# Performance work log

Hardware: AMD Instinct MI355X
Metric: run time of the kernel (lower is better)

## Reference

```python
import jax, jax.numpy as jnp
import numpy as np

N, DEG = 50000, 16
E = N * DEG
F_IN, HID, F_OUT, IJ = 128, 128, 128, 16


def _mlp2(x, W1, b1, W2, b2, tanh_out):
    y = jnp.tanh(x @ W1 + b1) @ W2 + b2
    return jnp.tanh(y) if tanh_out else y


def setup_inputs() -> dict:
    key = jax.random.key(0)
    ks = jax.random.split(key, 16)
    p = lambda k, sh: jax.random.normal(k, sh, dtype=jnp.float32) * 0.05
    inp = {
        "h": jax.random.normal(ks[0], (N, F_IN), dtype=jnp.float32),
        "x": jax.random.normal(ks[1], (N, 3), dtype=jnp.float32),
        "velocidade": jax.random.normal(ks[2], (N, 3), dtype=jnp.float32),
        "atributos_arestas": jax.random.normal(ks[3], (E, IJ), dtype=jnp.float32),
        "rows": jnp.repeat(jnp.arange(N, dtype=jnp.int32), DEG),
        "cols": jax.random.randint(ks[4], (E,), 0, N, dtype=jnp.int32),
        # phi_e: Linear(2F+1+IJ, HID), Tanh, Linear(HID, HID), Tanh
        "We1": p(ks[5], (2 * F_IN + 1 + IJ, HID)), "be1": jnp.zeros(HID, jnp.float32),
        "We2": p(ks[6], (HID, HID)), "be2": jnp.zeros(HID, jnp.float32),
        # phi_x: Linear(HID, HID), Tanh, Linear(HID, 1), Tanh
        "Wx1": p(ks[7], (HID, HID)), "bx1": jnp.zeros(HID, jnp.float32),
        "Wx2": p(ks[8], (HID, 1)), "bx2": jnp.zeros(1, jnp.float32),
        # phi_h: Linear(HID+1, HID), Tanh, Linear(HID, F_OUT)
        "Wh1": p(ks[9], (HID + 1, HID)), "bh1": jnp.zeros(HID, jnp.float32),
        "Wh2": p(ks[10], (HID, F_OUT)), "bh2": jnp.zeros(F_OUT, jnp.float32),
        # phi_v: Linear(F_IN, HID), Tanh, Linear(HID, 1)
        "Wv1": p(ks[11], (F_IN, HID)), "bv1": jnp.zeros(HID, jnp.float32),
        "Wv2": p(ks[12], (HID, 1)), "bv2": jnp.zeros(1, jnp.float32),
    }
    return inp


def reference(h, x, velocidade, atributos_arestas, rows, cols,
              We1, be1, We2, be2, Wx1, bx1, Wx2, bx2,
              Wh1, bh1, Wh2, bh2, Wv1, bv1, Wv2, bv2):
    n = h.shape[0]
    diff = x[rows] - x[cols]                              # [E, 3]
    dif_radial = jnp.sum(diff * diff, axis=1, keepdims=True)  # [E, 1]
    attrs = jnp.concatenate([h[rows], h[cols], dif_radial, atributos_arestas], axis=1)
    m_ij = _mlp2(attrs, We1, be1, We2, be2, tanh_out=True)    # [E, HID]
    phi_x = _mlp2(m_ij, Wx1, bx1, Wx2, bx2, tanh_out=True)    # [E, 1]
    phi_v = _mlp2(h, Wv1, bv1, Wv2, bv2, tanh_out=False)      # [N, 1]

    counts = jax.ops.segment_sum(jnp.ones_like(rows, dtype=diff.dtype), rows, num_segments=n)

    # media_segmentada: for edge (i=rows, j=cols): acc[i] += sum_over_features(edge_tensor[j])
    # (NOTE: indexes the EDGE tensor by the column NODE id j, faithful to source)
    ex = diff * phi_x                                     # [E, 3]
    vals = jnp.sum(ex[cols], axis=1)                      # [E]
    media = jax.ops.segment_sum(vals, rows, num_segments=n)
    media = jnp.where(counts > 0, media / counts, 0.0)[:, None]  # [N, 1]

    velocidade_new = velocidade * phi_v + media           # [N, 3]
    x_new = x + velocidade_new

    # soma_segmentada on m_ij with same quirky indexing
    m_vals = jnp.sum(m_ij[cols], axis=1)                  # [E]
    m_i = jax.ops.segment_sum(m_vals, rows, num_segments=n)[:, None]  # [N, 1]

    h_new = _mlp2(jnp.concatenate([h, m_i], axis=1), Wh1, bh1, Wh2, bh2, tanh_out=False)
    return h_new, x_new, velocidade_new
```

## Files before the change

kernel.cpp:

```cpp
#include <hip/hip_runtime.h>
#include <hip/hip_bf16.h>

#define NN      50000
#define DEG     16
#define FDIM    128
#define ASTR    296
#define OSTR    136
#define OFF_WE1 0
#define OFF_WE2 36864
#define OFF_WX1 53248
#define OFF_WV1 69632
#define OFF_WH1 86016
#define OFF_WH2 102400
#define WS_SHORTS 118784

typedef short v8s  __attribute__((ext_vector_type(8)));
typedef short v4sh __attribute__((ext_vector_type(4)));
typedef short v2sh __attribute__((ext_vector_type(2)));
typedef float v4f  __attribute__((ext_vector_type(4)));

__device__ __forceinline__ float fast_tanh(float xv) {
    float ax = fabsf(xv);
    float e2 = __expf(2.0f * ax);
    float r  = 1.0f - 2.0f / (e2 + 1.0f);
    return copysignf(r, xv);
}

__device__ __forceinline__ short f2bf(float f) {
    union { float f; unsigned u; } a; a.f = f;
    unsigned r = a.u + 0x7fffu + ((a.u >> 16) & 1u);
    return (short)(unsigned short)(r >> 16);
}
__device__ __forceinline__ float bf2f(short s) {
    union { unsigned u; float f; } a; a.u = ((unsigned)(unsigned short)s) << 16;
    return a.f;
}

__device__ __forceinline__ float wave_reduce_add(float v) {
#pragma unroll
    for (int m = 32; m >= 1; m >>= 1) v += __shfl_xor(v, m, 64);
    return v;
}

template<int KSTEPS, int ASTRIDE, int KPAD>
__device__ __forceinline__ void mfma_acc(
    const short* A, const short* __restrict__ Wt, int l, int w, v4f acc[2][2])
{
    const int lm = l & 15, lk = l >> 4;
    const short* a0p = A + lm * ASTRIDE + lk * 8;
    const short* a1p = a0p + 16 * ASTRIDE;
    const short* b0p = Wt + (w * 32 + lm) * KPAD + lk * 8;
    const short* b1p = b0p + 16 * KPAD;
#pragma unroll
    for (int ks = 0; ks < KSTEPS; ++ks) {
        v8s a0 = *(const v8s*)(a0p + ks * 32);
        v8s a1 = *(const v8s*)(a1p + ks * 32);
        v8s b0 = *(const v8s*)(b0p + ks * 32);
        v8s b1 = *(const v8s*)(b1p + ks * 32);
        acc[0][0] = __builtin_amdgcn_mfma_f32_16x16x32_bf16(a0, b0, acc[0][0], 0, 0, 0);
        acc[1][0] = __builtin_amdgcn_mfma_f32_16x16x32_bf16(a1, b0, acc[1][0], 0, 0, 0);
        acc[0][1] = __builtin_amdgcn_mfma_f32_16x16x32_bf16(a0, b1, acc[0][1], 0, 0, 0);
        acc[1][1] = __builtin_amdgcn_mfma_f32_16x16x32_bf16(a1, b1, acc[1][1], 0, 0, 0);
    }
}

__device__ __forceinline__ void acc_zero(v4f acc[2][2]) {
    v4f z = {0.f, 0.f, 0.f, 0.f};
    acc[0][0] = z; acc[0][1] = z; acc[1][0] = z; acc[1][1] = z;
}

__device__ __forceinline__ void epi_to_lds(
    v4f acc[2][2], short* O, const float* __restrict__ b, int l, int w)
{
    const int rl = (l >> 4) * 4, cl = l & 15;
#pragma unroll
    for (int nt = 0; nt < 2; ++nt) {
        const int col = w * 32 + nt * 16 + cl;
        const float bias = b[col];
#pragma unroll
        for (int mt = 0; mt < 2; ++mt) {
#pragma unroll
            for (int r = 0; r < 4; ++r) {
                float v = fast_tanh(acc[mt][nt][r] + bias);
                O[(mt * 16 + rl + r) * OSTR + col] = f2bf(v);
            }
        }
    }
}

__global__ __launch_bounds__(256) void prep_weights(
    const float* __restrict__ We1, const float* __restrict__ We2,
    const float* __restrict__ Wx1, const float* __restrict__ Wv1,
    const float* __restrict__ Wh1, const float* __restrict__ Wh2,
    short* __restrict__ wbuf)
{
    int idx = blockIdx.x * 256 + threadIdx.x;
    if (idx < 128 * 288) {
        int c = idx / 288, k = idx % 288;
        wbuf[OFF_WE1 + idx] = (k < 273) ? f2bf(We1[k * FDIM + c]) : (short)0;
        return;
    }
    idx -= 128 * 288;
    if (idx < 5 * 16384) {
        int layer = idx / 16384, r = idx % 16384;
        int c = r / 128, k = r % 128;
        const float* W = (layer == 0) ? We2 : (layer == 1) ? Wx1 :
                         (layer == 2) ? Wv1 : (layer == 3) ? Wh1 : Wh2;
        wbuf[OFF_WE2 + layer * 16384 + c * 128 + k] = f2bf(W[k * FDIM + c]);
    }
}

__global__ __launch_bounds__(256) void edge_kernel(
    const float* __restrict__ h, const float* __restrict__ x,
    const float* __restrict__ ea, const int* __restrict__ cols,
    const short* __restrict__ wbuf,
    const float* __restrict__ be1, const float* __restrict__ be2,
    const float* __restrict__ bx1,
    const float* __restrict__ Wx2, const float* __restrict__ bx2,
    float* __restrict__ msum, float* __restrict__ exsum)
{
    __shared__ __align__(16) short attrs[32 * ASTR];
    __shared__ __align__(16) short buf1[32 * OSTR];
    __shared__ __align__(16) short buf2[32 * OSTR];
    __shared__ float sdiff[32];

    const int tid = threadIdx.x;
    const int e0  = blockIdx.x * 32;
    const int l   = tid & 63, w = tid >> 6, eb = w * 8;

    {
        const int el = tid >> 3, q = tid & 7;
        int ec = e0 + el; if (ec >= NN) ec = NN - 1;
        const int i = ec >> 4;
        const int j = cols[ec];
        const float4* hi4 = (const float4*)(h + (size_t)i * FDIM);
        const float4* hj4 = (const float4*)(h + (size_t)j * FDIM);
        short* arow = attrs + el * ASTR;
#pragma unroll
        for (int t = 0; t < 4; ++t) {
            float4 v = hi4[q * 4 + t];
            v4sh s = { f2bf(v.x), f2bf(v.y), f2bf(v.z), f2bf(v.w) };
            *(v4sh*)(arow + q * 16 + t * 4) = s;
            float4 u = hj4[q * 4 + t];
            v4sh s2 = { f2bf(u.x), f2bf(u.y), f2bf(u.z), f2bf(u.w) };
            *(v4sh*)(arow + 128 + q * 16 + t * 4) = s2;
        }
        if (q < 2) {
#pragma unroll
            for (int t = 0; t < 8; ++t)
                arow[257 + q * 8 + t] = f2bf(ea[(size_t)ec * 16 + q * 8 + t]);
        }
        if (q == 2) {
            float dx = x[i * 3 + 0] - x[j * 3 + 0];
            float dy = x[i * 3 + 1] - x[j * 3 + 1];
            float dz = x[i * 3 + 2] - x[j * 3 + 2];
            arow[256] = f2bf(dx * dx + dy * dy + dz * dz);
            sdiff[el] = dx + dy + dz;
        }
        if (q == 3) {
#pragma unroll
            for (int t = 0; t < 15; ++t) arow[273 + t] = 0;
        }
    }
    __syncthreads();

    v4f acc[2][2];
    acc_zero(acc);
    mfma_acc<9, ASTR, 288>(attrs, wbuf + OFF_WE1, l, w, acc);
    epi_to_lds(acc, buf1, be1, l, w);
    __syncthreads();

    acc_zero(acc);
    mfma_acc<4, OSTR, 128>(buf1, wbuf + OFF_WE2, l, w, acc);
    epi_to_lds(acc, buf2, be2, l, w);
    __syncthreads();

#pragma unroll
    for (int e = 0; e < 8; ++e) {
        int row = eb + e;
        v2sh p = *(const v2sh*)(buf2 + row * OSTR + 2 * l);
        float s = bf2f(p.x) + bf2f(p.y);
        s = wave_reduce_add(s);
        if (l == 0) {
            int eg = e0 + row;
            if (eg < NN) msum[eg] = s;
        }
    }

    acc_zero(acc);
    mfma_acc<4, OSTR, 128>(buf2, wbuf + OFF_WX1, l, w, acc);
    epi_to_lds(acc, buf1, bx1, l, w);
    __syncthreads();

    {
        const float wx0 = Wx2[2 * l], wx1 = Wx2[2 * l + 1];
        const float bxx = bx2[0];
#pragma unroll
        for (int e = 0; e < 8; ++e) {
            int row = eb + e;
            v2sh p = *(const v2sh*)(buf1 + row * OSTR + 2 * l);
            float s = bf2f(p.x) * wx0 + bf2f(p.y) * wx1;
            s = wave_reduce_add(s);
            if (l == 0) {
                int eg = e0 + row;
                if (eg < NN) exsum[eg] = fast_tanh(s + bxx) * sdiff[row];
            }
        }
    }
}

__global__ __launch_bounds__(256) void node_kernel(
    const float* __restrict__ h, const float* __restrict__ x,
    const float* __restrict__ vel, const int* __restrict__ cols,
    const short* __restrict__ wbuf,
    const float* __restrict__ bv1, const float* __restrict__ Wv2,
    const float* __restrict__ bv2,
    const float* __restrict__ bh1, const float* __restrict__ Wh1f,
    const float* __restrict__ bh2,
    const float* __restrict__ msum, const float* __restrict__ exsum,
    float* __restrict__ out_h, float* __restrict__ out_x, float* __restrict__ out_v)
{
    __shared__ __align__(16) short hn[32 * OSTR];
    __shared__ __align__(16) short buf1[32 * OSTR];
    __shared__ float mi[32], media[32], phiv[32];

    const int tid = threadIdx.x;
    const int n0  = blockIdx.x * 32;
    const int l   = tid & 63, w = tid >> 6, eb = w * 8;

    {
        const int el = tid >> 3, q = tid & 7;
        int nc = n0 + el; if (nc >= NN) nc = NN - 1;
        const float4* hr = (const float4*)(h + (size_t)nc * FDIM);
        short* arow = hn + el * OSTR;
#pragma unroll
        for (int t = 0; t < 4; ++t) {
            float4 v = hr[q * 4 + t];
            v4sh s = { f2bf(v.x), f2bf(v.y), f2bf(v.z), f2bf(v.w) };
            *(v4sh*)(arow + q * 16 + t * 4) = s;
        }
    }
    {
#pragma unroll
        for (int r = 0; r < 2; ++r) {
            int idx = tid + r * 256;
            int nl = idx >> 4, kk = idx & 15;
            int nc = n0 + nl; if (nc >= NN) nc = NN - 1;
            int c = cols[(size_t)nc * DEG + kk];
            float ms = msum[c];
            float ex = exsum[c];
#pragma unroll
            for (int m = 8; m >= 1; m >>= 1) {
                ms += __shfl_xor(ms, m, 64);
                ex += __shfl_xor(ex, m, 64);
            }
            if (kk == 0) { mi[nl] = ms; media[nl] = ex * (1.0f / 16.0f); }
        }
    }
    __syncthreads();

    v4f acc[2][2];
    acc_zero(acc);
    mfma_acc<4, OSTR, 128>(hn, wbuf + OFF_WV1, l, w, acc);
    epi_to_lds(acc, buf1, bv1, l, w);
    __syncthreads();

    {
        const float wv0 = Wv2[2 * l], wv1 = Wv2[2 * l + 1];
        const float bvv = bv2[0];
#pragma unroll
        for (int e = 0; e < 8; ++e) {
            int row = eb + e;
            v2sh p = *(const v2sh*)(buf1 + row * OSTR + 2 * l);
            float s = bf2f(p.x) * wv0 + bf2f(p.y) * wv1;
            s = wave_reduce_add(s);
            if (l == 0) phiv[row] = s + bvv;
        }
    }
    __syncthreads();

    acc_zero(acc);
    mfma_acc<4, OSTR, 128>(hn, wbuf + OFF_WH1, l, w, acc);
    {
        const int rl = (l >> 4) * 4, cl = l & 15;
        const float* w128 = Wh1f + (size_t)FDIM * FDIM;
#pragma unroll
        for (int nt = 0; nt < 2; ++nt) {
            const int col = w * 32 + nt * 16 + cl;
            const float bias = bh1[col], wr = w128[col];
#pragma unroll
            for (int mt = 0; mt < 2; ++mt) {
#pragma unroll
                for (int r = 0; r < 4; ++r) {
                    int row = mt * 16 + rl + r;
                    float v = fast_tanh(acc[mt][nt][r] + bias + mi[row] * wr);
                    buf1[row * OSTR + col] = f2bf(v);
                }
            }
        }
    }
    __syncthreads();

    acc_zero(acc);
    mfma_acc<4, OSTR, 128>(buf1, wbuf + OFF_WH2, l, w, acc);
    {
        const int rl = (l >> 4) * 4, cl = l & 15;
#pragma unroll
        for (int nt = 0; nt < 2; ++nt) {
            const int col = w * 32 + nt * 16 + cl;
            const float bias = bh2[col];
#pragma unroll
            for (int mt = 0; mt < 2; ++mt) {
#pragma unroll
                for (int r = 0; r < 4; ++r) {
                    int rg = n0 + mt * 16 + rl + r;
                    if (rg < NN) out_h[(size_t)rg * FDIM + col] = acc[mt][nt][r] + bias;
                }
            }
        }
    }

    if (tid < 96) {
        int nl = tid / 3, d = tid % 3;
        int n = n0 + nl;
        if (n < NN) {
            float vv = vel[(size_t)n * 3 + d] * phiv[nl] + media[nl];
            out_v[(size_t)n * 3 + d] = vv;
            out_x[(size_t)n * 3 + d] = x[(size_t)n * 3 + d] + vv;
        }
    }
}

extern "C" void kernel_launch(void* const* d_in, const int* in_sizes, int n_in,
                              void* d_out, int out_size, void* d_ws, size_t ws_size,
                              hipStream_t stream)
{
    (void)in_sizes; (void)n_in; (void)out_size; (void)ws_size;
    const float* h    = (const float*)d_in[0];
    const float* x    = (const float*)d_in[1];
    const float* vel  = (const float*)d_in[2];
    const float* ea   = (const float*)d_in[3];
    const int*   cols = (const int*)d_in[5];
    const float* We1 = (const float*)d_in[6];  const float* be1 = (const float*)d_in[7];
    const float* We2 = (const float*)d_in[8];  const float* be2 = (const float*)d_in[9];
    const float* Wx1 = (const float*)d_in[10]; const float* bx1 = (const float*)d_in[11];
    const float* Wx2 = (const float*)d_in[12]; const float* bx2 = (const float*)d_in[13];
    const float* Wh1 = (const float*)d_in[14]; const float* bh1 = (const float*)d_in[15];
    const float* Wh2 = (const float*)d_in[16]; const float* bh2 = (const float*)d_in[17];
    const float* Wv1 = (const float*)d_in[18]; const float* bv1 = (const float*)d_in[19];
    const float* Wv2 = (const float*)d_in[20]; const float* bv2 = (const float*)d_in[21];

    short* wbuf  = (short*)d_ws;
    float* msum  = (float*)((char*)d_ws + WS_SHORTS * sizeof(short));
    float* exsum = msum + NN;
    float* out_h = (float*)d_out;
    float* out_x = out_h + (size_t)NN * FDIM;
    float* out_v = out_x + (size_t)NN * 3;

    dim3 block(256);
    prep_weights<<<dim3((WS_SHORTS + 255) / 256), block, 0, stream>>>(
        We1, We2, Wx1, Wv1, Wh1, Wh2, wbuf);
    dim3 grid((NN + 31) / 32);
    edge_kernel<<<grid, block, 0, stream>>>(h, x, ea, cols, wbuf,
                                            be1, be2, bx1, Wx2, bx2, msum, exsum);
    node_kernel<<<grid, block, 0, stream>>>(h, x, vel, cols, wbuf,
                                            bv1, Wv2, bv2, bh1, Wh1, bh2,
                                            msum, exsum, out_h, out_x, out_v);
}
```

Measured before the change: 212.8 us.

## Double row tile to 64 and hold weight fragments in registers

Each block now processes 64 rows instead of 32, and each wave preloads its B (weight) fragments into registers once per layer. The next layer's weights are fetched while the current layer's epilogue runs. This amortizes weight loads over more rows and cuts redundant global/LDS traffic. The attrs and second hidden buffer share LDS to limit shared memory growth. In exchange register pressure rises sharply (36 B fragments for the first layer) and the grid halves, which may reduce occupancy or parallelism.

```diff
diff --git a/kernel.cpp b/kernel.cpp
--- a/kernel.cpp
+++ b/kernel.cpp
@@ -4,6 +4,7 @@
 #define NN      50000
 #define DEG     16
 #define FDIM    128
+#define BM      64
 #define ASTR    296
 #define OSTR    136
 #define OFF_WE1 0
@@ -36,41 +37,47 @@
     return a.f;
 }
 
-__device__ __forceinline__ float wave_reduce_add(float v) {
-#pragma unroll
-    for (int m = 32; m >= 1; m >>= 1) v += __shfl_xor(v, m, 64);
-    return v;
-}
-
-template<int KSTEPS, int ASTRIDE, int KPAD>
-__device__ __forceinline__ void mfma_acc(
-    const short* A, const short* __restrict__ Wt, int l, int w, v4f acc[2][2])
+template<int KSTEPS, int KPAD>
+__device__ __forceinline__ void load_B(const short* __restrict__ Wt, int l, int w,
+                                       v8s B[KSTEPS][2])
 {
     const int lm = l & 15, lk = l >> 4;
-    const short* a0p = A + lm * ASTRIDE + lk * 8;
-    const short* a1p = a0p + 16 * ASTRIDE;
-    const short* b0p = Wt + (w * 32 + lm) * KPAD + lk * 8;
-    const short* b1p = b0p + 16 * KPAD;
+    const short* b0 = Wt + (size_t)(w * 32 + lm) * KPAD + lk * 8;
 #pragma unroll
     for (int ks = 0; ks < KSTEPS; ++ks) {
-        v8s a0 = *(const v8s*)(a0p + ks * 32);
-        v8s a1 = *(const v8s*)(a1p + ks * 32);
-        v8s b0 = *(const v8s*)(b0p + ks * 32);
-        v8s b1 = *(const v8s*)(b1p + ks * 32);
-        acc[0][0] = __builtin_amdgcn_mfma_f32_16x16x32_bf16(a0, b0, acc[0][0], 0, 0, 0);
-        acc[1][0] = __builtin_amdgcn_mfma_f32_16x16x32_bf16(a1, b0, acc[1][0], 0, 0, 0);
-        acc[0][1] = __builtin_amdgcn_mfma_f32_16x16x32_bf16(a0, b1, acc[0][1], 0, 0, 0);
-        acc[1][1] = __builtin_amdgcn_mfma_f32_16x16x32_bf16(a1, b1, acc[1][1], 0, 0, 0);
-    }
-}
-
-__device__ __forceinline__ void acc_zero(v4f acc[2][2]) {
+        B[ks][0] = *(const v8s*)(b0 + ks * 32);
+        B[ks][1] = *(const v8s*)(b0 + 16 * KPAD + ks * 32);
+    }
+}
+
+__device__ __forceinline__ void acc_zero(v4f acc[4][2]) {
     v4f z = {0.f, 0.f, 0.f, 0.f};
-    acc[0][0] = z; acc[0][1] = z; acc[1][0] = z; acc[1][1] = z;
-}
-
-__device__ __forceinline__ void epi_to_lds(
-    v4f acc[2][2], short* O, const float* __restrict__ b, int l, int w)
+#pragma unroll
+    for (int mt = 0; mt < 4; ++mt) { acc[mt][0] = z; acc[mt][1] = z; }
+}
+
+template<int KSTEPS, int ASTRIDE>
+__device__ __forceinline__ void mfma_acc(const short* A, const v8s B[KSTEPS][2],
+                                         int l, v4f acc[4][2])
+{
+    const int lm = l & 15, lk = l >> 4;
+    const short* ap = A + lm * ASTRIDE + lk * 8;
+#pragma unroll
+    for (int ks = 0; ks < KSTEPS; ++ks) {
+        v8s a[4];
+#pragma unroll
+        for (int mt = 0; mt < 4; ++mt)
+            a[mt] = *(const v8s*)(ap + mt * 16 * ASTRIDE + ks * 32);
+#pragma unroll
+        for (int mt = 0; mt < 4; ++mt) {
+            acc[mt][0] = __builtin_amdgcn_mfma_f32_16x16x32_bf16(a[mt], B[ks][0], acc[mt][0], 0, 0, 0);
+            acc[mt][1] = __builtin_amdgcn_mfma_f32_16x16x32_bf16(a[mt], B[ks][1], acc[mt][1], 0, 0, 0);
+        }
+    }
+}
+
+__device__ __forceinline__ void epi_to_lds(v4f acc[4][2], short* O,
+                                           const float* __restrict__ b, int l, int w)
 {
     const int rl = (l >> 4) * 4, cl = l & 15;
 #pragma unroll
@@ -78,13 +85,10 @@
         const int col = w * 32 + nt * 16 + cl;
         const float bias = b[col];
 #pragma unroll
-        for (int mt = 0; mt < 2; ++mt) {
-#pragma unroll
-            for (int r = 0; r < 4; ++r) {
-                float v = fast_tanh(acc[mt][nt][r] + bias);
-                O[(mt * 16 + rl + r) * OSTR + col] = f2bf(v);
-            }
-        }
+        for (int mt = 0; mt < 4; ++mt)
+#pragma unroll
+            for (int r = 0; r < 4; ++r)
+                O[(mt * 16 + rl + r) * OSTR + col] = f2bf(fast_tanh(acc[mt][nt][r] + bias));
     }
 }
 
@@ -110,7 +114,7 @@
     }
 }
 
-__global__ __launch_bounds__(256) void edge_kernel(
+__global__ __launch_bounds__(256, 2) void edge_kernel(
     const float* __restrict__ h, const float* __restrict__ x,
     const float* __restrict__ ea, const int* __restrict__ cols,
     const short* __restrict__ wbuf,
@@ -119,68 +123,78 @@
     const float* __restrict__ Wx2, const float* __restrict__ bx2,
     float* __restrict__ msum, float* __restrict__ exsum)
 {
-    __shared__ __align__(16) short attrs[32 * ASTR];
-    __shared__ __align__(16) short buf1[32 * OSTR];
-    __shared__ __align__(16) short buf2[32 * OSTR];
-    __shared__ float sdiff[32];
+    __shared__ __align__(16) short bigbuf[BM * ASTR];
+    __shared__ __align__(16) short buf1[BM * OSTR];
+    __shared__ float sdiff[BM];
+
+    short* attrs = bigbuf;
+    short* buf2  = bigbuf;
 
     const int tid = threadIdx.x;
-    const int e0  = blockIdx.x * 32;
-    const int l   = tid & 63, w = tid >> 6, eb = w * 8;
-
-    {
-        const int el = tid >> 3, q = tid & 7;
+    const int e0  = blockIdx.x * BM;
+    const int l   = tid & 63, w = tid >> 6;
+
+    v8s B1[9][2];
+    load_B<9, 288>(wbuf + OFF_WE1, l, w, B1);
+
+    {
+        const int el = tid >> 2, q = tid & 3;
         int ec = e0 + el; if (ec >= NN) ec = NN - 1;
         const int i = ec >> 4;
         const int j = cols[ec];
-        const float4* hi4 = (const float4*)(h + (size_t)i * FDIM);
-        const float4* hj4 = (const float4*)(h + (size_t)j * FDIM);
+        const float4* hi4 = (const float4*)(h + (size_t)i * FDIM) + q * 8;
+        const float4* hj4 = (const float4*)(h + (size_t)j * FDIM) + q * 8;
         short* arow = attrs + el * ASTR;
 #pragma unroll
-        for (int t = 0; t < 4; ++t) {
-            float4 v = hi4[q * 4 + t];
+        for (int t = 0; t < 8; ++t) {
+            float4 v = hi4[t];
             v4sh s = { f2bf(v.x), f2bf(v.y), f2bf(v.z), f2bf(v.w) };
-            *(v4sh*)(arow + q * 16 + t * 4) = s;
-            float4 u = hj4[q * 4 + t];
+            *(v4sh*)(arow + q * 32 + t * 4) = s;
+            float4 u = hj4[t];
             v4sh s2 = { f2bf(u.x), f2bf(u.y), f2bf(u.z), f2bf(u.w) };
-            *(v4sh*)(arow + 128 + q * 16 + t * 4) = s2;
-        }
-        if (q < 2) {
-#pragma unroll
-            for (int t = 0; t < 8; ++t)
-                arow[257 + q * 8 + t] = f2bf(ea[(size_t)ec * 16 + q * 8 + t]);
-        }
-        if (q == 2) {
+            *(v4sh*)(arow + 128 + q * 32 + t * 4) = s2;
+        }
+        if (q == 0) {
+#pragma unroll
+            for (int t = 0; t < 16; ++t)
+                arow[257 + t] = f2bf(ea[(size_t)ec * 16 + t]);
+        }
+        if (q == 1) {
             float dx = x[i * 3 + 0] - x[j * 3 + 0];
             float dy = x[i * 3 + 1] - x[j * 3 + 1];
             float dz = x[i * 3 + 2] - x[j * 3 + 2];
             arow[256] = f2bf(dx * dx + dy * dy + dz * dz);
             sdiff[el] = dx + dy + dz;
         }
-        if (q == 3) {
+        if (q == 2) {
 #pragma unroll
             for (int t = 0; t < 15; ++t) arow[273 + t] = 0;
         }
     }
     __syncthreads();
 
-    v4f acc[2][2];
-    acc_zero(acc);
-    mfma_acc<9, ASTR, 288>(attrs, wbuf + OFF_WE1, l, w, acc);
+    v4f acc[4][2];
+    acc_zero(acc);
+    mfma_acc<9, ASTR>(attrs, B1, l, acc);
+    v8s B2[4][2];
+    load_B<4, 128>(wbuf + OFF_WE2, l, w, B2);
     epi_to_lds(acc, buf1, be1, l, w);
     __syncthreads();
 
     acc_zero(acc);
-    mfma_acc<4, OSTR, 128>(buf1, wbuf + OFF_WE2, l, w, acc);
+    mfma_acc<4, OSTR>(buf1, B2, l, acc);
+    v8s B3[4][2];
+    load_B<4, 128>(wbuf + OFF_WX1, l, w, B3);
     epi_to_lds(acc, buf2, be2, l, w);
     __syncthreads();
 
 #pragma unroll
-    for (int e = 0; e < 8; ++e) {
-        int row = eb + e;
+    for (int e = 0; e < 16; ++e) {
+        int row = w * 16 + e;
         v2sh p = *(const v2sh*)(buf2 + row * OSTR + 2 * l);
         float s = bf2f(p.x) + bf2f(p.y);
-        s = wave_reduce_add(s);
+#pragma unroll
+        for (int m = 32; m >= 1; m >>= 1) s += __shfl_xor(s, m, 64);
         if (l == 0) {
             int eg = e0 + row;
             if (eg < NN) msum[eg] = s;
@@ -188,7 +202,7 @@
     }
 
     acc_zero(acc);
-    mfma_acc<4, OSTR, 128>(buf2, wbuf + OFF_WX1, l, w, acc);
+    mfma_acc<4, OSTR>(buf2, B3, l, acc);
     epi_to_lds(acc, buf1, bx1, l, w);
     __syncthreads();
 
@@ -196,11 +210,12 @@
         const float wx0 = Wx2[2 * l], wx1 = Wx2[2 * l + 1];
         const float bxx = bx2[0];
 #pragma unroll
-        for (int e = 0; e < 8; ++e) {
-            int row = eb + e;
+        for (int e = 0; e < 16; ++e) {
+            int row = w * 16 + e;
             v2sh p = *(const v2sh*)(buf1 + row * OSTR + 2 * l);
             float s = bf2f(p.x) * wx0 + bf2f(p.y) * wx1;
-            s = wave_reduce_add(s);
+#pragma unroll
+            for (int m = 32; m >= 1; m >>= 1) s += __shfl_xor(s, m, 64);
             if (l == 0) {
                 int eg = e0 + row;
                 if (eg < NN) exsum[eg] = fast_tanh(s + bxx) * sdiff[row];
@@ -209,7 +224,7 @@
     }
 }
 
-__global__ __launch_bounds__(256) void node_kernel(
+__global__ __launch_bounds__(256, 3) void node_kernel(
     const float* __restrict__ h, const float* __restrict__ x,
     const float* __restrict__ vel, const int* __restrict__ cols,
     const short* __restrict__ wbuf,
@@ -220,29 +235,33 @@
     const float* __restrict__ msum, const float* __restrict__ exsum,
     float* __restrict__ out_h, float* __restrict__ out_x, float* __restrict__ out_v)
 {
-    __shared__ __align__(16) short hn[32 * OSTR];
-    __shared__ __align__(16) short buf1[32 * OSTR];
-    __shared__ float mi[32], media[32], phiv[32];
+    __shared__ __align__(16) short hn[BM * OSTR];
+    __shared__ __align__(16) short buf1[BM * OSTR];
+    __shared__ float mi[BM], media[BM], phiv[BM];
 
     const int tid = threadIdx.x;
-    const int n0  = blockIdx.x * 32;
-    const int l   = tid & 63, w = tid >> 6, eb = w * 8;
-
-    {
-        const int el = tid >> 3, q = tid & 7;
+    const int n0  = blockIdx.x * BM;
+    const int l   = tid & 63, w = tid >> 6;
+
+    v8s B1[4][2], B2[4][2];
+    load_B<4, 128>(wbuf + OFF_WV1, l, w, B1);
+    load_B<4, 128>(wbuf + OFF_WH1, l, w, B2);
+
+    {
+        const int el = tid >> 2, q = tid & 3;
         int nc = n0 + el; if (nc >= NN) nc = NN - 1;
-        const float4* hr = (const float4*)(h + (size_t)nc * FDIM);
+        const float4* hr = (const float4*)(h + (size_t)nc * FDIM) + q * 8;
         short* arow = hn + el * OSTR;
 #pragma unroll
-        for (int t = 0; t < 4; ++t) {
-            float4 v = hr[q * 4 + t];
+        for (int t = 0; t < 8; ++t) {
+            float4 v = hr[t];
             v4sh s = { f2bf(v.x), f2bf(v.y), f2bf(v.z), f2bf(v.w) };
-            *(v4sh*)(arow + q * 16 + t * 4) = s;
-        }
-    }
-    {
-#pragma unroll
-        for (int r = 0; r < 2; ++r) {
+            *(v4sh*)(arow + q * 32 + t * 4) = s;
+        }
+    }
+    {
+#pragma unroll
+        for (int r = 0; r < 4; ++r) {
             int idx = tid + r * 256;
             int nl = idx >> 4, kk = idx & 15;
             int nc = n0 + nl; if (nc >= NN) nc = NN - 1;
@@ -259,9 +278,11 @@
     }
     __syncthreads();
 
-    v4f acc[2][2];
-    acc_zero(acc);
-    mfma_acc<4, OSTR, 128>(hn, wbuf + OFF_WV1, l, w, acc);
+    v4f acc[4][2];
+    acc_zero(acc);
+    mfma_acc<4, OSTR>(hn, B1, l, acc);
+    v8s B3[4][2];
+    load_B<4, 128>(wbuf + OFF_WH2, l, w, B3);
     epi_to_lds(acc, buf1, bv1, l, w);
     __syncthreads();
 
@@ -269,18 +290,19 @@
         const float wv0 = Wv2[2 * l], wv1 = Wv2[2 * l + 1];
         const float bvv = bv2[0];
 #pragma unroll
-        for (int e = 0; e < 8; ++e) {
-            int row = eb + e;
+        for (int e = 0; e < 16; ++e) {
+            int row = w * 16 + e;
             v2sh p = *(const v2sh*)(buf1 + row * OSTR + 2 * l);
             float s = bf2f(p.x) * wv0 + bf2f(p.y) * wv1;
-            s = wave_reduce_add(s);
+#pragma unroll
+            for (int m = 32; m >= 1; m >>= 1) s += __shfl_xor(s, m, 64);
             if (l == 0) phiv[row] = s + bvv;
         }
     }
     __syncthreads();
 
     acc_zero(acc);
-    mfma_acc<4, OSTR, 128>(hn, wbuf + OFF_WH1, l, w, acc);
+    mfma_acc<4, OSTR>(hn, B2, l, acc);
     {
         const int rl = (l >> 4) * 4, cl = l & 15;
         const float* w128 = Wh1f + (size_t)FDIM * FDIM;
@@ -289,20 +311,19 @@
             const int col = w * 32 + nt * 16 + cl;
             const float bias = bh1[col], wr = w128[col];
 #pragma unroll
-            for (int mt = 0; mt < 2; ++mt) {
+            for (int mt = 0; mt < 4; ++mt)
 #pragma unroll
                 for (int r = 0; r < 4; ++r) {
                     int row = mt * 16 + rl + r;
-                    float v = fast_tanh(acc[mt][nt][r] + bias + mi[row] * wr);
-                    buf1[row * OSTR + col] = f2bf(v);
+                    buf1[row * OSTR + col] =
+                        f2bf(fast_tanh(acc[mt][nt][r] + bias + mi[row] * wr));
                 }
-            }
-        }
-    }
-    __syncthreads();
-
-    acc_zero(acc);
-    mfma_acc<4, OSTR, 128>(buf1, wbuf + OFF_WH2, l, w, acc);
+        }
+    }
+    __syncthreads();
+
+    acc_zero(acc);
+    mfma_acc<4, OSTR>(buf1, B3, l, acc);
     {
         const int rl = (l >> 4) * 4, cl = l & 15;
 #pragma unroll
@@ -310,17 +331,16 @@
             const int col = w * 32 + nt * 16 + cl;
             const float bias = bh2[col];
 #pragma unroll
-            for (int mt = 0; mt < 2; ++mt) {
+            for (int mt = 0; mt < 4; ++mt)
 #pragma unroll
                 for (int r = 0; r < 4; ++r) {
                     int rg = n0 + mt * 16 + rl + r;
                     if (rg < NN) out_h[(size_t)rg * FDIM + col] = acc[mt][nt][r] + bias;
                 }
-            }
-        }
-    }
-
-    if (tid < 96) {
+        }
+    }
+
+    if (tid < BM * 3) {
         int nl = tid / 3, d = tid % 3;
         int n = n0 + nl;
         if (n < NN) {
@@ -360,7 +380,7 @@
     dim3 block(256);
     prep_weights<<<dim3((WS_SHORTS + 255) / 256), block, 0, stream>>>(
         We1, We2, Wx1, Wv1, Wh1, Wh2, wbuf);
-    dim3 grid((NN + 31) / 32);
+    dim3 grid((NN + BM - 1) / BM);
     edge_kernel<<<grid, block, 0, stream>>>(h, x, ea, cols, wbuf,
                                             be1, be2, bx1, Wx2, bx2, msum, exsum);
     node_kernel<<<grid, block, 0, stream>>>(h, x, vel, cols, wbuf,
```

Result: slower. 236.3 us (+11.0%).
